# Optimization experiments

Hardware: AMD Instinct MI355X
Metric: run time of the kernel (lower is better)

The kernel has to match this reference:

```python
import jax, jax.numpy as jnp
import numpy as np

N, F, D, H, L = 1536, 6, 64, 4, 2
DH = D // H
FF = 4 * D
EPS = 1e-5

def setup_inputs() -> dict:
    key = jax.random.key(0)
    ks = iter(jax.random.split(key, 32))
    def g(shape, scale=0.05):
        return jax.random.normal(next(ks), shape, jnp.float32) * scale
    return dict(
        node_feats=g((N, F), 1.0),
        proj_w=g((D, F)), proj_b=g((D,)),
        in_w=g((L, 3 * D, D)), in_b=g((L, 3 * D)),
        out_w=g((L, D, D)), out_b=g((L, D)),
        ff1_w=g((L, FF, D)), ff1_b=g((L, FF)),
        ff2_w=g((L, D, FF)), ff2_b=g((L, D)),
        ln1_g=jnp.ones((L, D), jnp.float32), ln1_b=jnp.zeros((L, D), jnp.float32),
        ln2_g=jnp.ones((L, D), jnp.float32), ln2_b=jnp.zeros((L, D), jnp.float32),
        ns_w=g((1, D)), ns_b=g((1,)),
        e1_w=g((D, 2 * D)), e1_b=g((D,)),
        e2_w=g((1, D)), e2_b=g((1,)),
    )

def _layernorm(x, g, b):
    mu = x.mean(-1, keepdims=True)
    var = ((x - mu) ** 2).mean(-1, keepdims=True)
    return (x - mu) / jnp.sqrt(var + EPS) * g + b

def _forward(node_feats, proj_w, proj_b, in_w, in_b, out_w, out_b,
             ff1_w, ff1_b, ff2_w, ff2_b, ln1_g, ln1_b, ln2_g, ln2_b,
             ns_w, ns_b, e1_w, e1_b, e2_w, e2_b):
    x = node_feats @ proj_w.T + proj_b  # (N, D)
    # Transformer encoder, post-norm, eval mode (dropout off); seq_len=N, batch=1.
    for l in range(L):
        qkv = x @ in_w[l].T + in_b[l]  # (N, 3D)
        q, k, v = jnp.split(qkv, 3, axis=-1)
        q = q.reshape(N, H, DH).transpose(1, 0, 2)  # (H, N, DH)
        k = k.reshape(N, H, DH).transpose(1, 0, 2)
        v = v.reshape(N, H, DH).transpose(1, 0, 2)
        scores = jnp.einsum('hnd,hmd->hnm', q, k) / jnp.sqrt(jnp.float32(DH))
        attn = jax.nn.softmax(scores, axis=-1)
        o = jnp.einsum('hnm,hmd->hnd', attn, v).transpose(1, 0, 2).reshape(N, D)
        sa = o @ out_w[l].T + out_b[l]
        x = _layernorm(x + sa, ln1_g[l], ln1_b[l])
        ff = jax.nn.relu(x @ ff1_w[l].T + ff1_b[l]) @ ff2_w[l].T + ff2_b[l]
        x = _layernorm(x + ff, ln2_g[l], ln2_b[l])
    node_logits = (x @ ns_w.T + ns_b)[:, 0]  # (N,)
    # Edge scoring: Linear(2D->D) on concat[x_i, x_j] == x_i @ A^T + x_j @ B^T + b1.
    # Precompute the two projections to avoid materializing the (N, N, 2D) concat.
    A, B = e1_w[:, :D], e1_w[:, D:]
    u = x @ A.T  # (N, D)
    w = x @ B.T  # (N, D)
    h = jax.nn.relu(u[:, None, :] + w[None, :, :] + e1_b)  # (N, N, D)
    edge_logits = jnp.einsum('nmd,d->nm', h, e2_w[0]) + e2_b[0]
    return node_logits, edge_logits

def reference(node_feats, proj_w, proj_b, in_w, in_b, out_w, out_b,
              ff1_w, ff1_b, ff2_w, ff2_b, ln1_g, ln1_b, ln2_g, ln2_b,
              ns_w, ns_b, e1_w, e1_b, e2_w, e2_b):
    return _forward(node_feats, proj_w, proj_b, in_w, in_b, out_w, out_b,
                    ff1_w, ff1_b, ff2_w, ff2_b, ln1_g, ln1_b, ln2_g, ln2_b,
                    ns_w, ns_b, e1_w, e1_b, e2_w, e2_b)
```

## Files before the change

kernel.cpp:

```cpp
#include <hip/hip_runtime.h>
#include <hip/hip_bf16.h>

#define N 1536
#define F 6
#define D 64
#define H 4
#define DH 16
#define FFDIM 256
#define NL 2
#define EPS 1e-5f
#define KS 4
#define KB (N / KS)
#define KW (KB / 4)

static __device__ __forceinline__ float dot4(float4 a, float4 b) {
    return a.x * b.x + a.y * b.y + a.z * b.z + a.w * b.w;
}

__global__ __launch_bounds__(192) void k_qkv0(const float* __restrict__ nf,
                                              const float* __restrict__ pw,
                                              const float* __restrict__ pb,
                                              const float* __restrict__ w,
                                              const float* __restrict__ b,
                                              float* __restrict__ x,
                                              float* __restrict__ qkv) {
    __shared__ __align__(16) float sx[8][D];
    int n0 = blockIdx.x * 8;
    int t = threadIdx.x;
    for (int i = t; i < 8 * D; i += 192) {
        int r = i >> 6, d = i & 63;
        float acc = pb[d];
#pragma unroll
        for (int f = 0; f < F; ++f) acc += nf[(n0 + r) * F + f] * pw[d * F + f];
        sx[r][d] = acc;
        x[(n0 + r) * D + d] = acc;
    }
    __syncthreads();
    const float4* wr = (const float4*)(w + t * D);
    float acc[8];
    float bb = b[t];
#pragma unroll
    for (int r = 0; r < 8; ++r) acc[r] = bb;
#pragma unroll
    for (int e = 0; e < D / 4; ++e) {
        float4 wv = wr[e];
#pragma unroll
        for (int r = 0; r < 8; ++r) acc[r] += dot4(wv, *(const float4*)&sx[r][e * 4]);
    }
#pragma unroll
    for (int r = 0; r < 8; ++r) qkv[(n0 + r) * (3 * D) + t] = acc[r];
}

__global__ __launch_bounds__(192) void k_qkv(const float* __restrict__ x,
                                             const float* __restrict__ w,
                                             const float* __restrict__ b,
                                             float* __restrict__ qkv) {
    __shared__ __align__(16) float sx[8][D];
    int n0 = blockIdx.x * 8;
    int t = threadIdx.x;
    if (t < 128) {
        int r = t >> 4, c4 = (t & 15) * 4;
        *(float4*)&sx[r][c4] = *(const float4*)&x[(n0 + r) * D + c4];
    }
    __syncthreads();
    const float4* wr = (const float4*)(w + t * D);
    float acc[8];
    float bb = b[t];
#pragma unroll
    for (int r = 0; r < 8; ++r) acc[r] = bb;
#pragma unroll
    for (int e = 0; e < D / 4; ++e) {
        float4 wv = wr[e];
#pragma unroll
        for (int r = 0; r < 8; ++r) acc[r] += dot4(wv, *(const float4*)&sx[r][e * 4]);
    }
#pragma unroll
    for (int r = 0; r < 8; ++r) qkv[(n0 + r) * (3 * D) + t] = acc[r];
}

struct SmemKV { float k[KB][DH]; float v[KB][DH]; };
struct SmemRed { float r[4][64][DH + 1]; };
__global__ __launch_bounds__(256) void k_attn_part(const float* __restrict__ qkv,
                                                   float* __restrict__ accp,
                                                   float* __restrict__ psump) {
    __shared__ __align__(16) union { SmemKV kv; SmemRed rd; } sm;
    int ks = blockIdx.x, qc = blockIdx.y, h = blockIdx.z;
    int t = threadIdx.x;
    int wv = t >> 6, lane = t & 63;

    for (int i = t; i < KB * 4; i += 256) {
        int row = i >> 2, c4 = (i & 3) * 4;
        const float* base = qkv + (size_t)(ks * KB + row) * (3 * D) + D + h * DH + c4;
        *(float4*)&sm.kv.k[row][c4] = *(const float4*)base;
        *(float4*)&sm.kv.v[row][c4] = *(const float4*)(base + D);
    }

    float q[DH];
    {
        const float4* qp = (const float4*)(qkv + (size_t)(qc * 64 + lane) * (3 * D) + h * DH);
#pragma unroll
        for (int e = 0; e < 4; ++e) {
            float4 v = qp[e];
            q[e * 4 + 0] = v.x * 0.25f;
            q[e * 4 + 1] = v.y * 0.25f;
            q[e * 4 + 2] = v.z * 0.25f;
            q[e * 4 + 3] = v.w * 0.25f;
        }
    }
    __syncthreads();

    float acc[DH];
#pragma unroll
    for (int i = 0; i < DH; ++i) acc[i] = 0.f;
    float psum = 0.f;

#pragma unroll 2
    for (int j = 0; j < KW; ++j) {
        int r = wv * KW + j;
        float4 k0 = *(const float4*)&sm.kv.k[r][0];
        float4 k1 = *(const float4*)&sm.kv.k[r][4];
        float4 k2 = *(const float4*)&sm.kv.k[r][8];
        float4 k3 = *(const float4*)&sm.kv.k[r][12];
        float s0 = q[0] * k0.x + q[1] * k0.y + q[2] * k0.z + q[3] * k0.w;
        float s1 = q[4] * k1.x + q[5] * k1.y + q[6] * k1.z + q[7] * k1.w;
        float s2 = q[8] * k2.x + q[9] * k2.y + q[10] * k2.z + q[11] * k2.w;
        float s3 = q[12] * k3.x + q[13] * k3.y + q[14] * k3.z + q[15] * k3.w;
        float p = __expf((s0 + s1) + (s2 + s3));
        psum += p;
        float4 v0 = *(const float4*)&sm.kv.v[r][0];
        float4 v1 = *(const float4*)&sm.kv.v[r][4];
        float4 v2 = *(const float4*)&sm.kv.v[r][8];
        float4 v3 = *(const float4*)&sm.kv.v[r][12];
        acc[0] += p * v0.x;  acc[1] += p * v0.y;  acc[2] += p * v0.z;  acc[3] += p * v0.w;
        acc[4] += p * v1.x;  acc[5] += p * v1.y;  acc[6] += p * v1.z;  acc[7] += p * v1.w;
        acc[8] += p * v2.x;  acc[9] += p * v2.y;  acc[10] += p * v2.z; acc[11] += p * v2.w;
        acc[12] += p * v3.x; acc[13] += p * v3.y; acc[14] += p * v3.z; acc[15] += p * v3.w;
    }

    __syncthreads();
#pragma unroll
    for (int i = 0; i < DH; ++i) sm.rd.r[wv][lane][i] = acc[i];
    sm.rd.r[wv][lane][DH] = psum;
    __syncthreads();

    for (int i = t; i < 64 * (DH + 1); i += 256) {
        int qq = i / (DH + 1), c = i % (DH + 1);
        float s = sm.rd.r[0][qq][c] + sm.rd.r[1][qq][c] + sm.rd.r[2][qq][c] + sm.rd.r[3][qq][c];
        int n = qc * 64 + qq;
        if (c < DH)
            accp[((size_t)ks * N + n) * D + h * DH + c] = s;
        else
            psump[((size_t)ks * N + n) * H + h] = s;
    }
}

__global__ __launch_bounds__(256) void k_attn_ffn(const float* __restrict__ accp,
                                                  const float* __restrict__ psump,
                                                  const float* __restrict__ ow,
                                                  const float* __restrict__ ob,
                                                  const float* __restrict__ g1,
                                                  const float* __restrict__ be1,
                                                  const float* __restrict__ w1,
                                                  const float* __restrict__ b1,
                                                  const float* __restrict__ w2,
                                                  const float* __restrict__ b2,
                                                  const float* __restrict__ g2,
                                                  const float* __restrict__ be2,
                                                  float* __restrict__ x) {
    __shared__ __align__(16) float so[4][D];
    __shared__ __align__(16) float sx[4][D];
    __shared__ __align__(16) float sh[4][FFDIM];
    __shared__ float sp[4][4][D];
    int t = threadIdx.x;
    int r = t >> 6, e = t & 63;
    int n = blockIdx.x * 4 + r;

    {
        float a = 0.f, p = 0.f;
#pragma unroll
        for (int ks = 0; ks < KS; ++ks) {
            a += accp[((size_t)ks * N + n) * D + e];
            p += psump[((size_t)ks * N + n) * H + (e >> 4)];
        }
        so[r][e] = a / p;
    }
    __syncthreads();

    {
        const float4* ir = (const float4*)so[r];
        const float4* wr = (const float4*)(ow + e * D);
        float acc = ob[e];
#pragma unroll
        for (int k = 0; k < D / 4; ++k) acc += dot4(ir[k], wr[k]);
        float y = x[n * D + e] + acc;
        float mu = y;
#pragma unroll
        for (int off = 32; off; off >>= 1) mu += __shfl_xor(mu, off, 64);
        mu *= (1.f / 64.f);
        float diff = y - mu;
        float var = diff * diff;
#pragma unroll
        for (int off = 32; off; off >>= 1) var += __shfl_xor(var, off, 64);
        var *= (1.f / 64.f);
        sx[r][e] = diff * rsqrtf(var + EPS) * g1[e] + be1[e];
    }
    __syncthreads();

    {
        const float4* wr = (const float4*)(w1 + t * D);
        float acc[4];
        float bb = b1[t];
#pragma unroll
        for (int rr = 0; rr < 4; ++rr) acc[rr] = bb;
#pragma unroll
        for (int k = 0; k < D / 4; ++k) {
            float4 wv = wr[k];
#pragma unroll
            for (int rr = 0; rr < 4; ++rr) acc[rr] += dot4(wv, *(const float4*)&sx[rr][k * 4]);
        }
#pragma unroll
        for (int rr = 0; rr < 4; ++rr) sh[rr][t] = fmaxf(acc[rr], 0.f);
    }
    __syncthreads();

    {
        int d = t & 63, c = t >> 6;
        const float4* wr = (const float4*)(w2 + d * FFDIM + c * 64);
        float acc[4] = {0.f, 0.f, 0.f, 0.f};
#pragma unroll
        for (int k = 0; k < 16; ++k) {
            float4 wv = wr[k];
#pragma unroll
            for (int rr = 0; rr < 4; ++rr) acc[rr] += dot4(wv, *(const float4*)&sh[rr][c * 64 + k * 4]);
        }
#pragma unroll
        for (int rr = 0; rr < 4; ++rr) sp[rr][c][d] = acc[rr];
    }
    __syncthreads();

    {
        float y = sx[r][e] + b2[e] + sp[r][0][e] + sp[r][1][e] + sp[r][2][e] + sp[r][3][e];
        float mu = y;
#pragma unroll
        for (int off = 32; off; off >>= 1) mu += __shfl_xor(mu, off, 64);
        mu *= (1.f / 64.f);
        float diff = y - mu;
        float var = diff * diff;
#pragma unroll
        for (int off = 32; off; off >>= 1) var += __shfl_xor(var, off, 64);
        var *= (1.f / 64.f);
        x[n * D + e] = diff * rsqrtf(var + EPS) * g2[e] + be2[e];
    }
}

__global__ __launch_bounds__(256) void k_node_uw(const float* __restrict__ x,
                                                 const float* __restrict__ nsw,
                                                 const float* __restrict__ nsb,
                                                 const float* __restrict__ e1w,
                                                 const float* __restrict__ e1b,
                                                 float* __restrict__ nodeo,
                                                 float* __restrict__ u,
                                                 float* __restrict__ wv) {
    __shared__ __align__(16) float sx[4][D];
    int t = threadIdx.x;
    int r = t >> 6, d = t & 63;
    int n = blockIdx.x * 4 + r;
    if (t < 64) {
        int rr = t >> 4, c4 = (t & 15) * 4;
        *(float4*)&sx[rr][c4] = *(const float4*)&x[(blockIdx.x * 4 + rr) * D + c4];
    }
    __syncthreads();
    const float4* xr = (const float4*)sx[r];
    const float4* ar = (const float4*)(e1w + d * 2 * D);
    const float4* br = (const float4*)(e1w + d * 2 * D + D);
    float au = 0.f, aw = 0.f;
#pragma unroll
    for (int e = 0; e < D / 4; ++e) {
        float4 xv = xr[e], av = ar[e], bv = br[e];
        au += dot4(xv, av);
        aw += dot4(xv, bv);
    }
    u[n * D + d] = au + e1b[d];
    wv[n * D + d] = aw;
    float p = sx[r][d] * nsw[d];
#pragma unroll
    for (int off = 32; off; off >>= 1) p += __shfl_xor(p, off, 64);
    if (d == 0) nodeo[n] = p + nsb[0];
}

__global__ __launch_bounds__(256) void k_edge(const float* __restrict__ u,
                                              const float* __restrict__ w,
                                              const float* __restrict__ e2w,
                                              const float* __restrict__ e2b,
                                              float* __restrict__ out) {
    __shared__ __align__(16) float su[64][68];
    __shared__ __align__(16) float sw[64][68];
    __shared__ __align__(16) float sv[64];
    int tn = blockIdx.y * 64, tm = blockIdx.x * 64;
    int t = threadIdx.x;
    for (int i = t; i < 64 * 16; i += 256) {
        int r = i >> 4, c4 = (i & 15) * 4;
        *(float4*)&su[r][c4] = *(const float4*)&u[(tn + r) * D + c4];
        *(float4*)&sw[r][c4] = *(const float4*)&w[(tm + r) * D + c4];
    }
    if (t < 64) sv[t] = e2w[t];
    __syncthreads();
    float eb = e2b[0];
    int c0 = t & 15, r0 = t >> 4;

    float acc[4][4];
#pragma unroll
    for (int j = 0; j < 4; ++j)
#pragma unroll
        for (int k = 0; k < 4; ++k) acc[j][k] = 0.f;

#pragma unroll 4
    for (int e0 = 0; e0 < 64; e0 += 4) {
        float4 vv = *(const float4*)&sv[e0];
        float4 a[4], bb[4];
#pragma unroll
        for (int j = 0; j < 4; ++j) a[j] = *(const float4*)&su[r0 + 16 * j][e0];
#pragma unroll
        for (int k = 0; k < 4; ++k) bb[k] = *(const float4*)&sw[c0 + 16 * k][e0];
#pragma unroll
        for (int j = 0; j < 4; ++j)
#pragma unroll
            for (int k = 0; k < 4; ++k) {
                acc[j][k] += fmaxf(a[j].x + bb[k].x, 0.f) * vv.x;
                acc[j][k] += fmaxf(a[j].y + bb[k].y, 0.f) * vv.y;
                acc[j][k] += fmaxf(a[j].z + bb[k].z, 0.f) * vv.z;
                acc[j][k] += fmaxf(a[j].w + bb[k].w, 0.f) * vv.w;
            }
    }
#pragma unroll
    for (int j = 0; j < 4; ++j)
#pragma unroll
        for (int k = 0; k < 4; ++k)
            out[(size_t)(tn + r0 + 16 * j) * N + (tm + c0 + 16 * k)] = acc[j][k] + eb;
}

extern "C" void kernel_launch(void* const* d_in, const int* in_sizes, int n_in,
                              void* d_out, int out_size, void* d_ws, size_t ws_size,
                              hipStream_t stream) {
    const float* node_feats = (const float*)d_in[0];
    const float* proj_w = (const float*)d_in[1];
    const float* proj_b = (const float*)d_in[2];
    const float* in_w = (const float*)d_in[3];
    const float* in_b = (const float*)d_in[4];
    const float* out_w = (const float*)d_in[5];
    const float* out_b = (const float*)d_in[6];
    const float* ff1_w = (const float*)d_in[7];
    const float* ff1_b = (const float*)d_in[8];
    const float* ff2_w = (const float*)d_in[9];
    const float* ff2_b = (const float*)d_in[10];
    const float* ln1_g = (const float*)d_in[11];
    const float* ln1_b = (const float*)d_in[12];
    const float* ln2_g = (const float*)d_in[13];
    const float* ln2_b = (const float*)d_in[14];
    const float* ns_w = (const float*)d_in[15];
    const float* ns_b = (const float*)d_in[16];
    const float* e1_w = (const float*)d_in[17];
    const float* e1_b = (const float*)d_in[18];
    const float* e2_w = (const float*)d_in[19];
    const float* e2_b = (const float*)d_in[20];

    float* out = (float*)d_out;

    float* x = (float*)d_ws;
    float* qkv = x + N * D;
    float* accp = qkv + N * 3 * D;
    float* psump = accp + KS * N * D;
    float* u = psump + KS * N * H;
    float* wbuf = u + N * D;

    for (int l = 0; l < NL; ++l) {
        if (l == 0)
            k_qkv0<<<N / 8, 192, 0, stream>>>(node_feats, proj_w, proj_b,
                                              in_w, in_b, x, qkv);
        else
            k_qkv<<<N / 8, 192, 0, stream>>>(
                x, in_w + (size_t)l * 3 * D * D, in_b + (size_t)l * 3 * D, qkv);
        {
            dim3 grid(KS, N / 64, H);
            k_attn_part<<<grid, 256, 0, stream>>>(qkv, accp, psump);
        }
        k_attn_ffn<<<N / 4, 256, 0, stream>>>(
            accp, psump, out_w + (size_t)l * D * D, out_b + (size_t)l * D,
            ln1_g + (size_t)l * D, ln1_b + (size_t)l * D,
            ff1_w + (size_t)l * FFDIM * D, ff1_b + (size_t)l * FFDIM,
            ff2_w + (size_t)l * D * FFDIM, ff2_b + (size_t)l * D,
            ln2_g + (size_t)l * D, ln2_b + (size_t)l * D, x);
    }

    k_node_uw<<<N / 4, 256, 0, stream>>>(x, ns_w, ns_b, e1_w, e1_b, out, u, wbuf);
    {
        dim3 grid(N / 64, N / 64);
        k_edge<<<grid, 256, 0, stream>>>(u, wbuf, e2_w, e2_b, out + N);
    }
}
```

Baseline: 117.7 us.

## Register-block four queries per thread in attention and fuse node/edge projections into FFN

The attention partial kernel now has each thread handle four query rows, so every K/V row read from shared memory is reused four times. The key dimension is split into 16 chunks instead of 4. The in-block reduction across the four waves is removed: each wave writes its own partial sums directly, giving 64 partials that the FFN kernel sums. The separate node-score and u/w projection kernel is folded into the last layer's FFN kernel, saving one launch and one read of x. The trade-off is higher register pressure, more partial-buffer traffic and a longer reduction loop in the FFN kernel.

```diff
diff --git a/kernel.cpp b/kernel.cpp
--- a/kernel.cpp
+++ b/kernel.cpp
@@ -9,9 +9,11 @@
 #define FFDIM 256
 #define NL 2
 #define EPS 1e-5f
-#define KS 4
+#define KS 16
 #define KB (N / KS)
 #define KW (KB / 4)
+#define QB 256
+#define NPART (KS * 4)
 
 static __device__ __forceinline__ float dot4(float4 a, float4 b) {
     return a.x * b.x + a.y * b.y + a.z * b.z + a.w * b.w;
@@ -79,11 +81,10 @@
 }
 
 struct SmemKV { float k[KB][DH]; float v[KB][DH]; };
-struct SmemRed { float r[4][64][DH + 1]; };
-__global__ __launch_bounds__(256) void k_attn_part(const float* __restrict__ qkv,
-                                                   float* __restrict__ accp,
-                                                   float* __restrict__ psump) {
-    __shared__ __align__(16) union { SmemKV kv; SmemRed rd; } sm;
+__global__ __launch_bounds__(256, 2) void k_attn_part(const float* __restrict__ qkv,
+                                                      float* __restrict__ accp,
+                                                      float* __restrict__ psump) {
+    __shared__ __align__(16) SmemKV sm;
     int ks = blockIdx.x, qc = blockIdx.y, h = blockIdx.z;
     int t = threadIdx.x;
     int wv = t >> 6, lane = t & 63;
@@ -91,66 +92,77 @@
     for (int i = t; i < KB * 4; i += 256) {
         int row = i >> 2, c4 = (i & 3) * 4;
         const float* base = qkv + (size_t)(ks * KB + row) * (3 * D) + D + h * DH + c4;
-        *(float4*)&sm.kv.k[row][c4] = *(const float4*)base;
-        *(float4*)&sm.kv.v[row][c4] = *(const float4*)(base + D);
-    }
-
-    float q[DH];
-    {
-        const float4* qp = (const float4*)(qkv + (size_t)(qc * 64 + lane) * (3 * D) + h * DH);
+        *(float4*)&sm.k[row][c4] = *(const float4*)base;
+        *(float4*)&sm.v[row][c4] = *(const float4*)(base + D);
+    }
+
+    float q[4][DH];
+#pragma unroll
+    for (int j = 0; j < 4; ++j) {
+        const float4* qp =
+            (const float4*)(qkv + (size_t)(qc * QB + j * 64 + lane) * (3 * D) + h * DH);
 #pragma unroll
         for (int e = 0; e < 4; ++e) {
             float4 v = qp[e];
-            q[e * 4 + 0] = v.x * 0.25f;
-            q[e * 4 + 1] = v.y * 0.25f;
-            q[e * 4 + 2] = v.z * 0.25f;
-            q[e * 4 + 3] = v.w * 0.25f;
-        }
-    }
-    __syncthreads();
-
-    float acc[DH];
-#pragma unroll
-    for (int i = 0; i < DH; ++i) acc[i] = 0.f;
-    float psum = 0.f;
+            q[j][e * 4 + 0] = v.x * 0.25f;
+            q[j][e * 4 + 1] = v.y * 0.25f;
+            q[j][e * 4 + 2] = v.z * 0.25f;
+            q[j][e * 4 + 3] = v.w * 0.25f;
+        }
+    }
+    __syncthreads();
+
+    float acc[4][DH];
+#pragma unroll
+    for (int j = 0; j < 4; ++j)
+#pragma unroll
+        for (int i = 0; i < DH; ++i) acc[j][i] = 0.f;
+    float psum[4] = {0.f, 0.f, 0.f, 0.f};
 
 #pragma unroll 2
-    for (int j = 0; j < KW; ++j) {
-        int r = wv * KW + j;
-        float4 k0 = *(const float4*)&sm.kv.k[r][0];
-        float4 k1 = *(const float4*)&sm.kv.k[r][4];
-        float4 k2 = *(const float4*)&sm.kv.k[r][8];
-        float4 k3 = *(const float4*)&sm.kv.k[r][12];
-        float s0 = q[0] * k0.x + q[1] * k0.y + q[2] * k0.z + q[3] * k0.w;
-        float s1 = q[4] * k1.x + q[5] * k1.y + q[6] * k1.z + q[7] * k1.w;
-        float s2 = q[8] * k2.x + q[9] * k2.y + q[10] * k2.z + q[11] * k2.w;
-        float s3 = q[12] * k3.x + q[13] * k3.y + q[14] * k3.z + q[15] * k3.w;
-        float p = __expf((s0 + s1) + (s2 + s3));
-        psum += p;
-        float4 v0 = *(const float4*)&sm.kv.v[r][0];
-        float4 v1 = *(const float4*)&sm.kv.v[r][4];
-        float4 v2 = *(const float4*)&sm.kv.v[r][8];
-        float4 v3 = *(const float4*)&sm.kv.v[r][12];
-        acc[0] += p * v0.x;  acc[1] += p * v0.y;  acc[2] += p * v0.z;  acc[3] += p * v0.w;
-        acc[4] += p * v1.x;  acc[5] += p * v1.y;  acc[6] += p * v1.z;  acc[7] += p * v1.w;
-        acc[8] += p * v2.x;  acc[9] += p * v2.y;  acc[10] += p * v2.z; acc[11] += p * v2.w;
-        acc[12] += p * v3.x; acc[13] += p * v3.y; acc[14] += p * v3.z; acc[15] += p * v3.w;
-    }
-
-    __syncthreads();
-#pragma unroll
-    for (int i = 0; i < DH; ++i) sm.rd.r[wv][lane][i] = acc[i];
-    sm.rd.r[wv][lane][DH] = psum;
-    __syncthreads();
-
-    for (int i = t; i < 64 * (DH + 1); i += 256) {
-        int qq = i / (DH + 1), c = i % (DH + 1);
-        float s = sm.rd.r[0][qq][c] + sm.rd.r[1][qq][c] + sm.rd.r[2][qq][c] + sm.rd.r[3][qq][c];
-        int n = qc * 64 + qq;
-        if (c < DH)
-            accp[((size_t)ks * N + n) * D + h * DH + c] = s;
-        else
-            psump[((size_t)ks * N + n) * H + h] = s;
+    for (int jk = 0; jk < KW; ++jk) {
+        int r = wv * KW + jk;
+        float4 k0 = *(const float4*)&sm.k[r][0];
+        float4 k1 = *(const float4*)&sm.k[r][4];
+        float4 k2 = *(const float4*)&sm.k[r][8];
+        float4 k3 = *(const float4*)&sm.k[r][12];
+        float p[4];
+#pragma unroll
+        for (int j = 0; j < 4; ++j) {
+            float s = q[j][0] * k0.x + q[j][1] * k0.y + q[j][2] * k0.z + q[j][3] * k0.w
+                    + q[j][4] * k1.x + q[j][5] * k1.y + q[j][6] * k1.z + q[j][7] * k1.w
+                    + q[j][8] * k2.x + q[j][9] * k2.y + q[j][10] * k2.z + q[j][11] * k2.w
+                    + q[j][12] * k3.x + q[j][13] * k3.y + q[j][14] * k3.z + q[j][15] * k3.w;
+            p[j] = __expf(s);
+            psum[j] += p[j];
+        }
+        float4 v0 = *(const float4*)&sm.v[r][0];
+        float4 v1 = *(const float4*)&sm.v[r][4];
+        float4 v2 = *(const float4*)&sm.v[r][8];
+        float4 v3 = *(const float4*)&sm.v[r][12];
+#pragma unroll
+        for (int j = 0; j < 4; ++j) {
+            acc[j][0] += p[j] * v0.x;  acc[j][1] += p[j] * v0.y;
+            acc[j][2] += p[j] * v0.z;  acc[j][3] += p[j] * v0.w;
+            acc[j][4] += p[j] * v1.x;  acc[j][5] += p[j] * v1.y;
+            acc[j][6] += p[j] * v1.z;  acc[j][7] += p[j] * v1.w;
+            acc[j][8] += p[j] * v2.x;  acc[j][9] += p[j] * v2.y;
+            acc[j][10] += p[j] * v2.z; acc[j][11] += p[j] * v2.w;
+            acc[j][12] += p[j] * v3.x; acc[j][13] += p[j] * v3.y;
+            acc[j][14] += p[j] * v3.z; acc[j][15] += p[j] * v3.w;
+        }
+    }
+
+    int part = ks * 4 + wv;
+#pragma unroll
+    for (int j = 0; j < 4; ++j) {
+        int n = qc * QB + j * 64 + lane;
+        float* ap = accp + ((size_t)part * N + n) * D + h * DH;
+        *(float4*)(ap + 0)  = make_float4(acc[j][0], acc[j][1], acc[j][2], acc[j][3]);
+        *(float4*)(ap + 4)  = make_float4(acc[j][4], acc[j][5], acc[j][6], acc[j][7]);
+        *(float4*)(ap + 8)  = make_float4(acc[j][8], acc[j][9], acc[j][10], acc[j][11]);
+        *(float4*)(ap + 12) = make_float4(acc[j][12], acc[j][13], acc[j][14], acc[j][15]);
+        psump[((size_t)part * N + n) * H + h] = psum[j];
     }
 }
 
@@ -166,7 +178,15 @@
                                                   const float* __restrict__ b2,
                                                   const float* __restrict__ g2,
                                                   const float* __restrict__ be2,
-                                                  float* __restrict__ x) {
+                                                  float* __restrict__ x,
+                                                  int tail,
+                                                  const float* __restrict__ nsw,
+                                                  const float* __restrict__ nsb,
+                                                  const float* __restrict__ e1w,
+                                                  const float* __restrict__ e1b,
+                                                  float* __restrict__ nodeo,
+                                                  float* __restrict__ u,
+                                                  float* __restrict__ wbuf) {
     __shared__ __align__(16) float so[4][D];
     __shared__ __align__(16) float sx[4][D];
     __shared__ __align__(16) float sh[4][FFDIM];
@@ -177,10 +197,10 @@
 
     {
         float a = 0.f, p = 0.f;
-#pragma unroll
-        for (int ks = 0; ks < KS; ++ks) {
-            a += accp[((size_t)ks * N + n) * D + e];
-            p += psump[((size_t)ks * N + n) * H + (e >> 4)];
+#pragma unroll 8
+        for (int pp = 0; pp < NPART; ++pp) {
+            a += accp[((size_t)pp * N + n) * D + e];
+            p += psump[((size_t)pp * N + n) * H + (e >> 4)];
         }
         so[r][e] = a / p;
     }
@@ -231,7 +251,8 @@
         for (int k = 0; k < 16; ++k) {
             float4 wv = wr[k];
 #pragma unroll
-            for (int rr = 0; rr < 4; ++rr) acc[rr] += dot4(wv, *(const float4*)&sh[rr][c * 64 + k * 4]);
+            for (int rr = 0; rr < 4; ++rr)
+                acc[rr] += dot4(wv, *(const float4*)&sh[rr][c * 64 + k * 4]);
         }
 #pragma unroll
         for (int rr = 0; rr < 4; ++rr) sp[rr][c][d] = acc[rr];
@@ -249,43 +270,32 @@
 #pragma unroll
         for (int off = 32; off; off >>= 1) var += __shfl_xor(var, off, 64);
         var *= (1.f / 64.f);
-        x[n * D + e] = diff * rsqrtf(var + EPS) * g2[e] + be2[e];
-    }
-}
-
-__global__ __launch_bounds__(256) void k_node_uw(const float* __restrict__ x,
-                                                 const float* __restrict__ nsw,
-                                                 const float* __restrict__ nsb,
-                                                 const float* __restrict__ e1w,
-                                                 const float* __restrict__ e1b,
-                                                 float* __restrict__ nodeo,
-                                                 float* __restrict__ u,
-                                                 float* __restrict__ wv) {
-    __shared__ __align__(16) float sx[4][D];
-    int t = threadIdx.x;
-    int r = t >> 6, d = t & 63;
-    int n = blockIdx.x * 4 + r;
-    if (t < 64) {
-        int rr = t >> 4, c4 = (t & 15) * 4;
-        *(float4*)&sx[rr][c4] = *(const float4*)&x[(blockIdx.x * 4 + rr) * D + c4];
-    }
-    __syncthreads();
-    const float4* xr = (const float4*)sx[r];
-    const float4* ar = (const float4*)(e1w + d * 2 * D);
-    const float4* br = (const float4*)(e1w + d * 2 * D + D);
-    float au = 0.f, aw = 0.f;
-#pragma unroll
-    for (int e = 0; e < D / 4; ++e) {
-        float4 xv = xr[e], av = ar[e], bv = br[e];
-        au += dot4(xv, av);
-        aw += dot4(xv, bv);
-    }
-    u[n * D + d] = au + e1b[d];
-    wv[n * D + d] = aw;
-    float p = sx[r][d] * nsw[d];
-#pragma unroll
-    for (int off = 32; off; off >>= 1) p += __shfl_xor(p, off, 64);
-    if (d == 0) nodeo[n] = p + nsb[0];
+        float xv = diff * rsqrtf(var + EPS) * g2[e] + be2[e];
+        x[n * D + e] = xv;
+        sx[r][e] = xv;
+    }
+
+    if (!tail) return;
+    __syncthreads();
+
+    {
+        const float4* xr = (const float4*)sx[r];
+        const float4* ar = (const float4*)(e1w + e * 2 * D);
+        const float4* br = (const float4*)(e1w + e * 2 * D + D);
+        float au = 0.f, aw = 0.f;
+#pragma unroll
+        for (int k = 0; k < D / 4; ++k) {
+            float4 xv = xr[k], av = ar[k], bv = br[k];
+            au += dot4(xv, av);
+            aw += dot4(xv, bv);
+        }
+        u[n * D + e] = au + e1b[e];
+        wbuf[n * D + e] = aw;
+        float p = sx[r][e] * nsw[e];
+#pragma unroll
+        for (int off = 32; off; off >>= 1) p += __shfl_xor(p, off, 64);
+        if (e == 0) nodeo[n] = p + nsb[0];
+    }
 }
 
 __global__ __launch_bounds__(256) void k_edge(const float* __restrict__ u,
@@ -369,8 +379,8 @@
     float* x = (float*)d_ws;
     float* qkv = x + N * D;
     float* accp = qkv + N * 3 * D;
-    float* psump = accp + KS * N * D;
-    float* u = psump + KS * N * H;
+    float* psump = accp + (size_t)NPART * N * D;
+    float* u = psump + (size_t)NPART * N * H;
     float* wbuf = u + N * D;
 
     for (int l = 0; l < NL; ++l) {
@@ -381,7 +391,7 @@
             k_qkv<<<N / 8, 192, 0, stream>>>(
                 x, in_w + (size_t)l * 3 * D * D, in_b + (size_t)l * 3 * D, qkv);
         {
-            dim3 grid(KS, N / 64, H);
+            dim3 grid(KS, N / QB, H);
             k_attn_part<<<grid, 256, 0, stream>>>(qkv, accp, psump);
         }
         k_attn_ffn<<<N / 4, 256, 0, stream>>>(
@@ -389,10 +399,10 @@
             ln1_g + (size_t)l * D, ln1_b + (size_t)l * D,
             ff1_w + (size_t)l * FFDIM * D, ff1_b + (size_t)l * FFDIM,
             ff2_w + (size_t)l * D * FFDIM, ff2_b + (size_t)l * D,
-            ln2_g + (size_t)l * D, ln2_b + (size_t)l * D, x);
-    }
-
-    k_node_uw<<<N / 4, 256, 0, stream>>>(x, ns_w, ns_b, e1_w, e1_b, out, u, wbuf);
+            ln2_g + (size_t)l * D, ln2_b + (size_t)l * D, x,
+            (l == NL - 1) ? 1 : 0, ns_w, ns_b, e1_w, e1_b, out, u, wbuf);
+    }
+
     {
         dim3 grid(N / 64, N / 64);
         k_edge<<<grid, 256, 0, stream>>>(u, wbuf, e2_w, e2_b, out + N);
```

Measured after the change: 142.0 us. +20.6%, slower.
